# Performance work log

Measured on AMD Instinct MI355X. Metric: run time of the kernel, lower is better.

The kernel has to match this reference:

```python
import jax, jax.numpy as jnp
import numpy as np

DIM = 128
N_PROMPT = 5
N_EXPERTS = 4
TOP_K = 2
HIDDEN = int(DIM * 2.66)  # 340
LOSS_COEF = 1e-2
EPS = 1e-10


def setup_inputs() -> dict:
    key = jax.random.key(0)
    ks = jax.random.split(key, 12)
    B, C, H, W = 2, DIM, 192, 192
    s = 0.02
    return {
        "x": jax.random.normal(ks[0], (B, C, H, W), jnp.float32),
        "prompt": jax.random.normal(ks[1], (N_PROMPT, DIM), jnp.float32) * s,      # spectral_prompt
        "w_lin": jax.random.normal(ks[2], (N_PROMPT, DIM), jnp.float32) * s,       # Linear(dim, 5).weight
        "b_lin": jnp.zeros((N_PROMPT,), jnp.float32),
        "w_conv": jax.random.normal(ks[3], (DIM, DIM), jnp.float32) * s,           # Conv2d 1x1, no bias
        "w_gate": jax.random.normal(ks[4], (DIM, N_EXPERTS), jnp.float32) * s,     # gating matrix
        "w1": jax.random.normal(ks[5], (N_EXPERTS, DIM, HIDDEN), jnp.float32) * s, # expert fc1
        "b1": jnp.zeros((N_EXPERTS, HIDDEN), jnp.float32),
        "w2": jax.random.normal(ks[6], (N_EXPERTS, HIDDEN, DIM), jnp.float32) * s, # expert fc2
        "b2": jnp.zeros((N_EXPERTS, DIM), jnp.float32),
    }


def _cv_squared(v):
    # coefficient of variation squared: var / mean^2
    m = jnp.mean(v)
    return jnp.var(v) / (m * m + EPS)


def _moe(tx, ty, w_gate, w1, b1, w2, b2):
    # tx: [N, C] gating input tokens; ty: [N, C] expert input tokens
    logits = tx @ w_gate                                  # [N, E] (clean gating, inference path)
    top_logits, top_idx = jax.lax.top_k(logits, TOP_K)    # [N, k]
    top_gates = jax.nn.softmax(top_logits, axis=-1)       # [N, k]
    N = tx.shape[0]
    gates = jnp.zeros((N, N_EXPERTS), tx.dtype).at[
        jnp.arange(N)[:, None], top_idx].set(top_gates)   # [N, E] sparse gates
    importance = gates.sum(axis=0)                        # [E]
    load = (gates > 0).astype(tx.dtype).sum(axis=0)       # [E]
    loss = LOSS_COEF * (_cv_squared(importance) + _cv_squared(load))
    # dense masked dispatch: run every expert, weight-combine (same math as routed combine)
    h = jax.nn.gelu(jnp.einsum('nc,ech->enh', ty, w1) + b1[:, None, :], approximate=False)
    o = jnp.einsum('enh,ehc->enc', h, w2) + b2[:, None, :]  # [E, N, C]
    y = jnp.einsum('ne,enc->nc', gates, o)                  # [N, C]
    return y, loss


def reference(x, prompt, w_lin, b_lin, w_conv, w_gate, w1, b1, w2, b2):
    B, C, H, W = x.shape
    emb = x.mean(axis=(-2, -1))                               # [B, C]
    pw = jax.nn.softmax(emb @ w_lin.T + b_lin, axis=1)        # [B, P]
    spectral_prompt = pw @ prompt                             # [B, C]
    sf = spectral_prompt[:, :, None, None] * x                # [B, C, H, W]
    out = jnp.einsum('oc,bchw->bohw', w_conv, sf)             # 1x1 conv, no bias
    tx = jnp.transpose(x, (0, 2, 3, 1)).reshape(-1, C)        # gating tokens
    ty = jnp.transpose(out, (0, 2, 3, 1)).reshape(-1, C)      # expert tokens
    y, loss = _moe(tx, ty, w_gate, w1, b1, w2, b2)
    y = jnp.transpose(y.reshape(B, H, W, C), (0, 3, 1, 2))
    return y + x, loss
```

## Files before the change

### kernel.cpp

```cpp
#include <hip/hip_runtime.h>
#include <hip/hip_bf16.h>
#include <hip/hip_fp8.h>

typedef __attribute__((ext_vector_type(8))) short bf16x8;
typedef __attribute__((ext_vector_type(4))) float f32x4;
typedef long long i64;
typedef __attribute__((ext_vector_type(2))) long long i64x2;

#define HW 36864
#define HID 340
#define HPAD 352
#define ECP 1408
#define NCHUNK 44
#define TILE 96
#define TILES_PER_B 384
#define OUT_Y_ELEMS 9437184
#define WALL_BYTES (NCHUNK * 8192)

__device__ __forceinline__ short f2bf(float f) {
    __hip_bfloat16 h = __float2bfloat16(f);
    union { __hip_bfloat16 h; short s; } u; u.h = h; return u.s;
}
__device__ __forceinline__ float bf2f(short s) {
    union { unsigned u; float f; } v; v.u = ((unsigned)(unsigned short)s) << 16; return v.f;
}
__device__ __forceinline__ f32x4 mfma_fp8(i64 a, i64 b, f32x4 c) {
    return __builtin_amdgcn_mfma_f32_16x16x32_fp8_fp8(a, b, c, 0, 0, 0);
}
__device__ __forceinline__ void async_cp16(const void* gsrc, void* ldst) {
    __builtin_amdgcn_global_load_lds(
        (const __attribute__((address_space(1))) unsigned int*)gsrc,
        (__attribute__((address_space(3))) unsigned int*)ldst, 16, 0, 0);
}

__global__ __launch_bounds__(256) void k_prep(const float* __restrict__ x,
                                              const float* __restrict__ w1, const float* __restrict__ w2,
                                              const float* __restrict__ b1,
                                              float* __restrict__ emb, unsigned char* __restrict__ Wall,
                                              float* __restrict__ b1c) {
    int blk = blockIdx.x;
    int tid = threadIdx.x;
    if (blk < 256) {
        const float* p = x + (size_t)blk * HW;
        float s = 0.f;
        for (int i = tid * 4; i < HW; i += 1024) {
            float4 v = *(const float4*)(p + i);
            s += v.x + v.y + v.z + v.w;
        }
        for (int off = 32; off; off >>= 1) s += __shfl_down(s, off);
        __shared__ float wsum[4];
        int lane = tid & 63, wid = tid >> 6;
        if (lane == 0) wsum[wid] = s;
        __syncthreads();
        if (tid == 0) emb[blk] = (wsum[0] + wsum[1] + wsum[2] + wsum[3]) * (1.f / (float)HW);
        return;
    }
    if (blk < 608) {
        int idx4 = (blk - 256) * 1024 + tid * 4;
        int ch = idx4 >> 13, r8 = idx4 & 8191;
        int rr = r8 >> 10;
        int lane = (r8 >> 4) & 63;
        int j0 = r8 & 15;
        int g16 = lane >> 4, l16 = lane & 15;
        int jj0 = j0 & 7;
        float v0 = 0.f, v1 = 0.f, v2 = 0.f, v3 = 0.f;
        if (rr < 4) {
            int m = rr >> 1, p = rr & 1;
            int kk = 2 * p + (j0 >> 3);
            int j_h = ch * 32 + m * 16 + l16;
            int c0 = 16 * (2 * kk + (jj0 >> 2)) + 4 * g16;
            int e = j_h / HPAD, h = j_h - e * HPAD;
            if (h < HID) {
                const float* p1 = w1 + ((size_t)(e * 128 + c0)) * HID + h;
                v0 = p1[0] * 32.f; v1 = p1[HID] * 32.f; v2 = p1[2 * HID] * 32.f; v3 = p1[3 * HID] * 32.f;
            }
        } else {
            int q = rr - 4;
            int oc = 2 * q + (j0 >> 3);
            int o = oc * 16 + l16;
            int jg0 = ch * 32 + 16 * (jj0 >> 2) + 4 * g16;
            int e = jg0 / HPAD, h = jg0 - e * HPAD;
            if (h < HID) {
                const float* p2 = w2 + ((size_t)(e * HID + h)) * 128 + o;
                v0 = p2[0] * 32.f; v1 = p2[128] * 32.f; v2 = p2[256] * 32.f; v3 = p2[384] * 32.f;
            }
        }
        unsigned w = __builtin_amdgcn_cvt_pk_fp8_f32(v0, v1, 0, false);
        w = __builtin_amdgcn_cvt_pk_fp8_f32(v2, v3, w, true);
        *(unsigned*)(Wall + idx4) = w;
        return;
    }
    {
        int j0 = (blk - 608) * 1024 + tid * 4;
        if (j0 < ECP) {
            int e = j0 / HPAD, h = j0 - e * HPAD;
            float4 o;
            if (h < HID) {
                const float* p = b1 + e * HID + h;
                o.x = p[0]; o.y = p[1]; o.z = p[2]; o.w = p[3];
            } else {
                o.x = o.y = o.z = o.w = 0.f;
            }
            *(float4*)(b1c + j0) = o;
        }
    }
}

__global__ __launch_bounds__(256) void k_wb(const float* __restrict__ emb, const float* __restrict__ prompt,
                                            const float* __restrict__ wlin, const float* __restrict__ blin,
                                            const float* __restrict__ wconv,
                                            short* __restrict__ WbBf, float* __restrict__ stat) {
    __shared__ float lp[2][5];
    __shared__ float pw[2][5];
    __shared__ float sv[2][128];
    int tid = threadIdx.x;
    if (tid < 10) {
        int b = tid / 5, p = tid % 5;
        float s = blin[p];
        for (int c = 0; c < 128; ++c) s += emb[b * 128 + c] * wlin[p * 128 + c];
        lp[b][p] = s;
    }
    __syncthreads();
    if (tid < 2) {
        float m = lp[tid][0];
        for (int p = 1; p < 5; ++p) m = fmaxf(m, lp[tid][p]);
        float e[5], sum = 0.f;
        for (int p = 0; p < 5; ++p) { e[p] = __expf(lp[tid][p] - m); sum += e[p]; }
        for (int p = 0; p < 5; ++p) pw[tid][p] = e[p] / sum;
    }
    __syncthreads();
    {
        int b = tid >> 7, c = tid & 127;
        float s = 0.f;
        for (int p = 0; p < 5; ++p) s += pw[b][p] * prompt[p * 128 + c];
        sv[b][c] = s;
    }
    __syncthreads();
    int i0 = blockIdx.x * 1024 + tid * 4;
    int b = i0 >> 14, o = (i0 >> 7) & 127, c = i0 & 127;
    float4 wv = *(const float4*)(wconv + o * 128 + c);
    short r0 = f2bf(wv.x * sv[b][c]);
    short r1 = f2bf(wv.y * sv[b][c + 1]);
    short r2 = f2bf(wv.z * sv[b][c + 2]);
    short r3 = f2bf(wv.w * sv[b][c + 3]);
    WbBf[i0] = r0; WbBf[i0 + 1] = r1; WbBf[i0 + 2] = r2; WbBf[i0 + 3] = r3;
    if (blockIdx.x == 0 && tid < 8) stat[tid] = 0.f;
}

__global__ __launch_bounds__(192, 3) void k_main(
    const float* __restrict__ x, const float* __restrict__ wgate, const float* __restrict__ b2,
    const short* __restrict__ WbBf, const unsigned char* __restrict__ Wall,
    const float* __restrict__ b1c, float* __restrict__ stat, float* __restrict__ out) {

    __shared__ __align__(16) unsigned char uni[26112];
    __shared__ __align__(16) short b1sh[ECP];
    __shared__ float gates[TILE][4];
    __shared__ float simp[4], sload[4];
    short (*Xs)[136] = (short (*)[136])uni;
    unsigned char (*ring)[8192] = (unsigned char (*)[8192])uni;

    int tid = threadIdx.x;
    int tb = blockIdx.x;
    int b = tb / TILES_PER_B;
    int hw0 = (tb % TILES_PER_B) * TILE;
    const float* xb = x + (size_t)b * 128 * HW + hw0;

    int lane = tid & 63, wid = tid >> 6;
    int g16 = lane >> 4, l16 = lane & 15;
    int wrow = wid * 32;

    if (tid < 4) { simp[tid] = 0.f; sload[tid] = 0.f; }
    for (int i = tid; i < ECP; i += 192) b1sh[i] = f2bf(b1c[i]);

    #pragma unroll
    for (int it = 0; it < 16; ++it) {
        int i = tid + it * 192;
        int c = i / 24;
        int k = i - c * 24;
        float4 v = *(const float4*)(xb + (size_t)c * HW + k * 4);
        int t = k * 4;
        Xs[t][c] = f2bf(v.x); Xs[t + 1][c] = f2bf(v.y);
        Xs[t + 2][c] = f2bf(v.z); Xs[t + 3][c] = f2bf(v.w);
    }
    __syncthreads();

    bf16x8 xf[2][4];
    #pragma unroll
    for (int nt = 0; nt < 2; ++nt)
        #pragma unroll
        for (int kk = 0; kk < 4; ++kk)
            xf[nt][kk] = *(const bf16x8*)&Xs[wrow + nt * 16 + l16][kk * 32 + g16 * 8];

    {
        bf16x8 wgA[4];
        #pragma unroll
        for (int kk = 0; kk < 4; ++kk) {
            bf16x8 a = (bf16x8){0, 0, 0, 0, 0, 0, 0, 0};
            if (l16 < 4) {
                #pragma unroll
                for (int jj = 0; jj < 8; ++jj)
                    a[jj] = f2bf(wgate[(kk * 32 + g16 * 8 + jj) * 4 + l16]);
            }
            wgA[kk] = a;
        }
        f32x4 lg0 = (f32x4){0.f, 0.f, 0.f, 0.f};
        f32x4 lg1 = (f32x4){0.f, 0.f, 0.f, 0.f};
        #pragma unroll
        for (int kk = 0; kk < 4; ++kk) {
            lg0 = __builtin_amdgcn_mfma_f32_16x16x32_bf16(wgA[kk], xf[0][kk], lg0, 0, 0, 0);
            lg1 = __builtin_amdgcn_mfma_f32_16x16x32_bf16(wgA[kk], xf[1][kk], lg1, 0, 0, 0);
        }
        if (g16 == 0) {
            #pragma unroll
            for (int nt = 0; nt < 2; ++nt) {
                f32x4 lg = nt ? lg1 : lg0;
                float l0 = lg[0], l1 = lg[1], l2 = lg[2], l3 = lg[3];
                int i1 = 0; float m1 = l0;
                if (l1 > m1) { m1 = l1; i1 = 1; }
                if (l2 > m1) { m1 = l2; i1 = 2; }
                if (l3 > m1) { m1 = l3; i1 = 3; }
                float m2 = -3.4e38f; int i2 = 0;
                if (i1 != 0) { m2 = l0; i2 = 0; }
                if (i1 != 1 && l1 > m2) { m2 = l1; i2 = 1; }
                if (i1 != 2 && l2 > m2) { m2 = l2; i2 = 2; }
                if (i1 != 3 && l3 > m2) { m2 = l3; i2 = 3; }
                float g2v = 1.f / (1.f + __expf(m1 - m2));
                float g1v = 1.f - g2v;
                int t = wrow + nt * 16 + l16;
                gates[t][0] = 0.f; gates[t][1] = 0.f; gates[t][2] = 0.f; gates[t][3] = 0.f;
                gates[t][i1] = g1v; gates[t][i2] = g2v;
                atomicAdd(&simp[i1], g1v); atomicAdd(&simp[i2], g2v);
                atomicAdd(&sload[i1], 1.f); atomicAdd(&sload[i2], 1.f);
            }
        }
    }

    f32x4 aty[2][8];
    #pragma unroll
    for (int nt = 0; nt < 2; ++nt)
        #pragma unroll
        for (int oc = 0; oc < 8; ++oc) aty[nt][oc] = (f32x4){0.f, 0.f, 0.f, 0.f};
    {
        const short* wbB = WbBf + b * 16384 + l16 * 128 + g16 * 8;
        #pragma unroll
        for (int oc = 0; oc < 8; ++oc) {
            #pragma unroll
            for (int kk = 0; kk < 4; ++kk) {
                bf16x8 wv = *(const bf16x8*)(wbB + oc * 16 * 128 + kk * 32);
                aty[0][oc] = __builtin_amdgcn_mfma_f32_16x16x32_bf16(wv, xf[0][kk], aty[0][oc], 0, 0, 0);
                aty[1][oc] = __builtin_amdgcn_mfma_f32_16x16x32_bf16(wv, xf[1][kk], aty[1][oc], 0, 0, 0);
            }
        }
    }
    i64 tyb8[2][4];
    #pragma unroll
    for (int nt = 0; nt < 2; ++nt)
        #pragma unroll
        for (int kk = 0; kk < 4; ++kk) {
            union { i64 l; unsigned u[2]; } uu;
            float v0 = aty[nt][2 * kk][0] * 64.f,     v1 = aty[nt][2 * kk][1] * 64.f;
            float v2 = aty[nt][2 * kk][2] * 64.f,     v3 = aty[nt][2 * kk][3] * 64.f;
            float v4 = aty[nt][2 * kk + 1][0] * 64.f, v5 = aty[nt][2 * kk + 1][1] * 64.f;
            float v6 = aty[nt][2 * kk + 1][2] * 64.f, v7 = aty[nt][2 * kk + 1][3] * 64.f;
            unsigned lo = __builtin_amdgcn_cvt_pk_fp8_f32(v0, v1, 0, false);
            lo = __builtin_amdgcn_cvt_pk_fp8_f32(v2, v3, lo, true);
            unsigned hi = __builtin_amdgcn_cvt_pk_fp8_f32(v4, v5, 0, false);
            hi = __builtin_amdgcn_cvt_pk_fp8_f32(v6, v7, hi, true);
            uu.u[0] = lo; uu.u[1] = hi;
            tyb8[nt][kk] = uu.l;
        }

    f32x4 gt0 = *(const f32x4*)&gates[wrow + l16][0];
    f32x4 gt1 = *(const f32x4*)&gates[wrow + 16 + l16][0];

    f32x4 accy[2][8];
    #pragma unroll
    for (int nt = 0; nt < 2; ++nt)
        #pragma unroll
        for (int oc = 0; oc < 8; ++oc) accy[nt][oc] = (f32x4){0.f, 0.f, 0.f, 0.f};

    __syncthreads();

    if (wid < 2) {
        const unsigned char* s0 = Wall + wid * 4096;
        #pragma unroll
        for (int r = 0; r < 4; ++r)
            async_cp16(s0 + r * 1024 + lane * 16, &ring[0][wid * 4096 + r * 1024 + lane * 16]);
        const unsigned char* s1 = Wall + 8192 + wid * 4096;
        #pragma unroll
        for (int r = 0; r < 4; ++r)
            async_cp16(s1 + r * 1024 + lane * 16, &ring[1][wid * 4096 + r * 1024 + lane * 16]);
    }

    int slot = 0;
    #pragma unroll 1
    for (int ch = 0; ch < NCHUNK; ++ch) {
        if (wid < 2) asm volatile("s_waitcnt vmcnt(4)" ::: "memory");
        __builtin_amdgcn_sched_barrier(0);
        __builtin_amdgcn_s_barrier();
        __builtin_amdgcn_sched_barrier(0);

        if (wid < 2) {
            int chn = (ch + 2 <= NCHUNK - 1) ? ch + 2 : NCHUNK - 1;
            int wslot = slot + 2; if (wslot >= 3) wslot -= 3;
            const unsigned char* src = Wall + (size_t)chn * 8192 + wid * 4096;
            unsigned char* dst = &ring[wslot][wid * 4096];
            #pragma unroll
            for (int r = 0; r < 4; ++r)
                async_cp16(src + r * 1024 + lane * 16, dst + r * 1024 + lane * 16);
        }

        const unsigned char* wst = &ring[slot][0];
        i64x2 f1q[2][2], f2q[4];
        f1q[0][0] = *(const i64x2*)(wst + 0 * 1024 + lane * 16);
        f1q[0][1] = *(const i64x2*)(wst + 1 * 1024 + lane * 16);
        f1q[1][0] = *(const i64x2*)(wst + 2 * 1024 + lane * 16);
        f1q[1][1] = *(const i64x2*)(wst + 3 * 1024 + lane * 16);
        f2q[0] = *(const i64x2*)(wst + 4 * 1024 + lane * 16);
        f2q[1] = *(const i64x2*)(wst + 5 * 1024 + lane * 16);
        f2q[2] = *(const i64x2*)(wst + 6 * 1024 + lane * 16);
        f2q[3] = *(const i64x2*)(wst + 7 * 1024 + lane * 16);

        int e4 = (ch >= 33) ? 3 : (ch >= 22) ? 2 : (ch >= 11) ? 1 : 0;
        float ge0 = (e4 == 0) ? gt0[0] : (e4 == 1) ? gt0[1] : (e4 == 2) ? gt0[2] : gt0[3];
        float ge1 = (e4 == 0) ? gt1[0] : (e4 == 1) ? gt1[1] : (e4 == 2) ? gt1[2] : gt1[3];

        f32x4 hacc[2][2];
        hacc[0][0] = (f32x4){0.f,0.f,0.f,0.f}; hacc[0][1] = (f32x4){0.f,0.f,0.f,0.f};
        hacc[1][0] = (f32x4){0.f,0.f,0.f,0.f}; hacc[1][1] = (f32x4){0.f,0.f,0.f,0.f};
        #pragma unroll
        for (int kk = 0; kk < 4; ++kk) {
            i64 a0 = f1q[0][kk >> 1][kk & 1];
            i64 a1 = f1q[1][kk >> 1][kk & 1];
            hacc[0][0] = mfma_fp8(a0, tyb8[0][kk], hacc[0][0]);
            hacc[0][1] = mfma_fp8(a0, tyb8[1][kk], hacc[0][1]);
            hacc[1][0] = mfma_fp8(a1, tyb8[0][kk], hacc[1][0]);
            hacc[1][1] = mfma_fp8(a1, tyb8[1][kk], hacc[1][1]);
        }

        float hv0[8], hv1[8];
        #pragma unroll
        for (int jc = 0; jc < 2; ++jc)
            #pragma unroll
            for (int rr = 0; rr < 4; ++rr) {
                float bv = bf2f(b1sh[ch * 32 + jc * 16 + 4 * g16 + rr]);
                float u0 = hacc[jc][0][rr] * 4.8828125e-4f + bv;
                float u1 = hacc[jc][1][rr] * 4.8828125e-4f + bv;
                hv0[jc * 4 + rr] = u0 * (1024.f + 816.9738f * u0) * ge0;
                hv1[jc * 4 + rr] = u1 * (1024.f + 816.9738f * u1) * ge1;
            }
        union { i64 l; unsigned u[2]; } f0, f1;
        {
            unsigned lo = __builtin_amdgcn_cvt_pk_fp8_f32(hv0[0], hv0[1], 0, false);
            lo = __builtin_amdgcn_cvt_pk_fp8_f32(hv0[2], hv0[3], lo, true);
            unsigned hi = __builtin_amdgcn_cvt_pk_fp8_f32(hv0[4], hv0[5], 0, false);
            hi = __builtin_amdgcn_cvt_pk_fp8_f32(hv0[6], hv0[7], hi, true);
            f0.u[0] = lo; f0.u[1] = hi;
            lo = __builtin_amdgcn_cvt_pk_fp8_f32(hv1[0], hv1[1], 0, false);
            lo = __builtin_amdgcn_cvt_pk_fp8_f32(hv1[2], hv1[3], lo, true);
            hi = __builtin_amdgcn_cvt_pk_fp8_f32(hv1[4], hv1[5], 0, false);
            hi = __builtin_amdgcn_cvt_pk_fp8_f32(hv1[6], hv1[7], hi, true);
            f1.u[0] = lo; f1.u[1] = hi;
        }

        #pragma unroll
        for (int oc = 0; oc < 8; ++oc) {
            i64 wv = f2q[oc >> 1][oc & 1];
            accy[0][oc] = mfma_fp8(wv, f0.l, accy[0][oc]);
            accy[1][oc] = mfma_fp8(wv, f1.l, accy[1][oc]);
        }

        slot = (slot == 2) ? 0 : slot + 1;
    }

    #pragma unroll
    for (int oc = 0; oc < 8; ++oc) {
        f32x4 b2v0 = *(const f32x4*)&b2[0 * 128 + oc * 16 + 4 * g16];
        f32x4 b2v1 = *(const f32x4*)&b2[1 * 128 + oc * 16 + 4 * g16];
        f32x4 b2v2 = *(const f32x4*)&b2[2 * 128 + oc * 16 + 4 * g16];
        f32x4 b2v3 = *(const f32x4*)&b2[3 * 128 + oc * 16 + 4 * g16];
        #pragma unroll
        for (int nt = 0; nt < 2; ++nt) {
            f32x4 gt = nt ? gt1 : gt0;
            #pragma unroll
            for (int r = 0; r < 4; ++r) {
                int o = oc * 16 + 4 * g16 + r;
                size_t addr = (size_t)(b * 128 + o) * HW + hw0 + wrow + nt * 16 + l16;
                float v = accy[nt][oc][r] * 1.52587890625e-5f
                        + gt[0] * b2v0[r] + gt[1] * b2v1[r] + gt[2] * b2v2[r] + gt[3] * b2v3[r]
                        + x[addr];
                out[addr] = v;
            }
        }
    }

    __syncthreads();
    if (tid < 4) {
        atomicAdd(&stat[tid], simp[tid]);
        atomicAdd(&stat[4 + tid], sload[tid]);
    }
}

__global__ void k_loss(const float* __restrict__ stat, float* __restrict__ out) {
    if (threadIdx.x == 0 && blockIdx.x == 0) {
        double mi = 0.0, ml = 0.0;
        for (int e = 0; e < 4; ++e) { mi += stat[e]; ml += stat[4 + e]; }
        mi *= 0.25; ml *= 0.25;
        double vi = 0.0, vl = 0.0;
        for (int e = 0; e < 4; ++e) {
            double di = stat[e] - mi; vi += di * di;
            double dl = stat[4 + e] - ml; vl += dl * dl;
        }
        vi *= 0.25; vl *= 0.25;
        out[OUT_Y_ELEMS] = (float)(0.01 * (vi / (mi * mi + 1e-10) + vl / (ml * ml + 1e-10)));
    }
}

extern "C" void kernel_launch(void* const* d_in, const int* in_sizes, int n_in,
                              void* d_out, int out_size, void* d_ws, size_t ws_size,
                              hipStream_t stream) {
    const float* x      = (const float*)d_in[0];
    const float* prompt = (const float*)d_in[1];
    const float* wlin   = (const float*)d_in[2];
    const float* blin   = (const float*)d_in[3];
    const float* wconv  = (const float*)d_in[4];
    const float* wgate  = (const float*)d_in[5];
    const float* w1     = (const float*)d_in[6];
    const float* b1     = (const float*)d_in[7];
    const float* w2     = (const float*)d_in[8];
    const float* b2     = (const float*)d_in[9];
    float* out = (float*)d_out;

    char* ws = (char*)d_ws;
    float* emb  = (float*)(ws + 0);
    float* stat = (float*)(ws + 1024);
    float* b1c  = (float*)(ws + 2048);
    short* WbBf = (short*)(ws + 8192);
    unsigned char* Wall = (unsigned char*)(ws + 73728);

    hipLaunchKernelGGL(k_prep, dim3(610),  dim3(256), 0, stream, x, w1, w2, b1, emb, Wall, b1c);
    hipLaunchKernelGGL(k_wb,   dim3(32),   dim3(256), 0, stream, emb, prompt, wlin, blin, wconv, WbBf, stat);
    hipLaunchKernelGGL(k_main, dim3(768),  dim3(192), 0, stream, x, wgate, b2, WbBf, Wall, b1c, stat, out);
    hipLaunchKernelGGL(k_loss, dim3(1),    dim3(1),   0, stream, stat, out);
}
```

Before: 94.06 us.

## Batch weight streaming into 32KB superchunks with double buffering and bias-in-accumulator

Restructures the weight pipeline from a 3-slot ring of 8KB chunks with one barrier per chunk to a 2-slot ring of 32KB superchunks, each covering four chunks. This cuts barriers and waits per unit of work by four. It also folds the fc1 bias, prescaled into fp32 LDS, into the MFMA accumulator initialisation, which removes per-element bias adds and bf16 conversions. The price is 64KB+ of LDS per block, so occupancy drops from 3 to 2 blocks per CU (launch bounds changed), and a second barrier per superchunk is needed before the buffer is refilled.

```diff
diff --git a/kernel.cpp b/kernel.cpp
--- a/kernel.cpp
+++ b/kernel.cpp
@@ -12,6 +12,7 @@
 #define HPAD 352
 #define ECP 1408
 #define NCHUNK 44
+#define NSUPER 11
 #define TILE 96
 #define TILES_PER_B 384
 #define OUT_Y_ELEMS 9437184
@@ -20,9 +21,6 @@
 __device__ __forceinline__ short f2bf(float f) {
     __hip_bfloat16 h = __float2bfloat16(f);
     union { __hip_bfloat16 h; short s; } u; u.h = h; return u.s;
-}
-__device__ __forceinline__ float bf2f(short s) {
-    union { unsigned u; float f; } v; v.u = ((unsigned)(unsigned short)s) << 16; return v.f;
 }
 __device__ __forceinline__ f32x4 mfma_fp8(i64 a, i64 b, f32x4 c) {
     return __builtin_amdgcn_mfma_f32_16x16x32_fp8_fp8(a, b, c, 0, 0, 0);
@@ -147,17 +145,77 @@
     if (blockIdx.x == 0 && tid < 8) stat[tid] = 0.f;
 }
 
-__global__ __launch_bounds__(192, 3) void k_main(
+#define SUB_BODY(CH, WST) do { \
+    int ch_ = (CH); \
+    const unsigned char* wst_ = (WST); \
+    i64x2 f1q[2][2], f2q[4]; \
+    f1q[0][0] = *(const i64x2*)(wst_ + 0 * 1024 + lane * 16); \
+    f1q[0][1] = *(const i64x2*)(wst_ + 1 * 1024 + lane * 16); \
+    f1q[1][0] = *(const i64x2*)(wst_ + 2 * 1024 + lane * 16); \
+    f1q[1][1] = *(const i64x2*)(wst_ + 3 * 1024 + lane * 16); \
+    f2q[0] = *(const i64x2*)(wst_ + 4 * 1024 + lane * 16); \
+    f2q[1] = *(const i64x2*)(wst_ + 5 * 1024 + lane * 16); \
+    f2q[2] = *(const i64x2*)(wst_ + 6 * 1024 + lane * 16); \
+    f2q[3] = *(const i64x2*)(wst_ + 7 * 1024 + lane * 16); \
+    int e4_ = (ch_ >= 33) ? 3 : (ch_ >= 22) ? 2 : (ch_ >= 11) ? 1 : 0; \
+    float ge0_ = (e4_ == 0) ? gt0[0] : (e4_ == 1) ? gt0[1] : (e4_ == 2) ? gt0[2] : gt0[3]; \
+    float ge1_ = (e4_ == 0) ? gt1[0] : (e4_ == 1) ? gt1[1] : (e4_ == 2) ? gt1[2] : gt1[3]; \
+    f32x4 bv0 = *(const f32x4*)&b1f[ch_ * 32 + 4 * g16]; \
+    f32x4 bv1 = *(const f32x4*)&b1f[ch_ * 32 + 16 + 4 * g16]; \
+    f32x4 hacc[2][2]; \
+    hacc[0][0] = bv0; hacc[0][1] = bv0; \
+    hacc[1][0] = bv1; hacc[1][1] = bv1; \
+    _Pragma("unroll") \
+    for (int kk = 0; kk < 4; ++kk) { \
+        i64 a0 = f1q[0][kk >> 1][kk & 1]; \
+        i64 a1 = f1q[1][kk >> 1][kk & 1]; \
+        hacc[0][0] = mfma_fp8(a0, tyb8[0][kk], hacc[0][0]); \
+        hacc[0][1] = mfma_fp8(a0, tyb8[1][kk], hacc[0][1]); \
+        hacc[1][0] = mfma_fp8(a1, tyb8[0][kk], hacc[1][0]); \
+        hacc[1][1] = mfma_fp8(a1, tyb8[1][kk], hacc[1][1]); \
+    } \
+    float hv0[8], hv1[8]; \
+    _Pragma("unroll") \
+    for (int jc = 0; jc < 2; ++jc) \
+        _Pragma("unroll") \
+        for (int rr = 0; rr < 4; ++rr) { \
+            float u0 = hacc[jc][0][rr] * 4.8828125e-4f; \
+            float u1 = hacc[jc][1][rr] * 4.8828125e-4f; \
+            hv0[jc * 4 + rr] = u0 * (1024.f + 816.9738f * u0) * ge0_; \
+            hv1[jc * 4 + rr] = u1 * (1024.f + 816.9738f * u1) * ge1_; \
+        } \
+    union { i64 l; unsigned u[2]; } f0, f1; \
+    { \
+        unsigned lo = __builtin_amdgcn_cvt_pk_fp8_f32(hv0[0], hv0[1], 0, false); \
+        lo = __builtin_amdgcn_cvt_pk_fp8_f32(hv0[2], hv0[3], lo, true); \
+        unsigned hi = __builtin_amdgcn_cvt_pk_fp8_f32(hv0[4], hv0[5], 0, false); \
+        hi = __builtin_amdgcn_cvt_pk_fp8_f32(hv0[6], hv0[7], hi, true); \
+        f0.u[0] = lo; f0.u[1] = hi; \
+        lo = __builtin_amdgcn_cvt_pk_fp8_f32(hv1[0], hv1[1], 0, false); \
+        lo = __builtin_amdgcn_cvt_pk_fp8_f32(hv1[2], hv1[3], lo, true); \
+        hi = __builtin_amdgcn_cvt_pk_fp8_f32(hv1[4], hv1[5], 0, false); \
+        hi = __builtin_amdgcn_cvt_pk_fp8_f32(hv1[6], hv1[7], hi, true); \
+        f1.u[0] = lo; f1.u[1] = hi; \
+    } \
+    _Pragma("unroll") \
+    for (int oc = 0; oc < 8; ++oc) { \
+        i64 wv = f2q[oc >> 1][oc & 1]; \
+        accy[0][oc] = mfma_fp8(wv, f0.l, accy[0][oc]); \
+        accy[1][oc] = mfma_fp8(wv, f1.l, accy[1][oc]); \
+    } \
+} while (0)
+
+__global__ __launch_bounds__(192, 2) void k_main(
     const float* __restrict__ x, const float* __restrict__ wgate, const float* __restrict__ b2,
     const short* __restrict__ WbBf, const unsigned char* __restrict__ Wall,
     const float* __restrict__ b1c, float* __restrict__ stat, float* __restrict__ out) {
 
-    __shared__ __align__(16) unsigned char uni[26112];
-    __shared__ __align__(16) short b1sh[ECP];
+    __shared__ __align__(16) unsigned char uni[65536];
+    __shared__ __align__(16) float b1f[ECP];
     __shared__ float gates[TILE][4];
     __shared__ float simp[4], sload[4];
     short (*Xs)[136] = (short (*)[136])uni;
-    unsigned char (*ring)[8192] = (unsigned char (*)[8192])uni;
+    unsigned char (*ring)[32768] = (unsigned char (*)[32768])uni;
 
     int tid = threadIdx.x;
     int tb = blockIdx.x;
@@ -170,7 +228,7 @@
     int wrow = wid * 32;
 
     if (tid < 4) { simp[tid] = 0.f; sload[tid] = 0.f; }
-    for (int i = tid; i < ECP; i += 192) b1sh[i] = f2bf(b1c[i]);
+    for (int i = tid; i < ECP; i += 192) b1f[i] = b1c[i] * 2048.f;
 
     #pragma unroll
     for (int it = 0; it < 16; ++it) {
@@ -282,95 +340,42 @@
     __syncthreads();
 
     if (wid < 2) {
-        const unsigned char* s0 = Wall + wid * 4096;
-        #pragma unroll
-        for (int r = 0; r < 4; ++r)
-            async_cp16(s0 + r * 1024 + lane * 16, &ring[0][wid * 4096 + r * 1024 + lane * 16]);
-        const unsigned char* s1 = Wall + 8192 + wid * 4096;
-        #pragma unroll
-        for (int r = 0; r < 4; ++r)
-            async_cp16(s1 + r * 1024 + lane * 16, &ring[1][wid * 4096 + r * 1024 + lane * 16]);
-    }
-
-    int slot = 0;
+        #pragma unroll
+        for (int r = 0; r < 16; ++r)
+            async_cp16(Wall + wid * 16384 + r * 1024 + lane * 16,
+                       &ring[0][wid * 16384 + r * 1024 + lane * 16]);
+        #pragma unroll
+        for (int r = 0; r < 16; ++r)
+            async_cp16(Wall + 32768 + wid * 16384 + r * 1024 + lane * 16,
+                       &ring[1][wid * 16384 + r * 1024 + lane * 16]);
+    }
+
     #pragma unroll 1
-    for (int ch = 0; ch < NCHUNK; ++ch) {
-        if (wid < 2) asm volatile("s_waitcnt vmcnt(4)" ::: "memory");
+    for (int s = 0; s < NSUPER; ++s) {
+        asm volatile("s_waitcnt vmcnt(16)" ::: "memory");
         __builtin_amdgcn_sched_barrier(0);
         __builtin_amdgcn_s_barrier();
         __builtin_amdgcn_sched_barrier(0);
 
+        const unsigned char* base = &ring[s & 1][0];
+        SUB_BODY(4 * s + 0, base);
+        SUB_BODY(4 * s + 1, base + 8192);
+        SUB_BODY(4 * s + 2, base + 16384);
+        SUB_BODY(4 * s + 3, base + 24576);
+
+        asm volatile("s_waitcnt lgkmcnt(0)" ::: "memory");
+        __builtin_amdgcn_sched_barrier(0);
+        __builtin_amdgcn_s_barrier();
+        __builtin_amdgcn_sched_barrier(0);
+
         if (wid < 2) {
-            int chn = (ch + 2 <= NCHUNK - 1) ? ch + 2 : NCHUNK - 1;
-            int wslot = slot + 2; if (wslot >= 3) wslot -= 3;
-            const unsigned char* src = Wall + (size_t)chn * 8192 + wid * 4096;
-            unsigned char* dst = &ring[wslot][wid * 4096];
+            int sn = (s + 2 <= NSUPER - 1) ? s + 2 : NSUPER - 1;
+            const unsigned char* src = Wall + (size_t)sn * 32768 + wid * 16384;
+            unsigned char* dst = &ring[s & 1][wid * 16384];
             #pragma unroll
-            for (int r = 0; r < 4; ++r)
+            for (int r = 0; r < 16; ++r)
                 async_cp16(src + r * 1024 + lane * 16, dst + r * 1024 + lane * 16);
         }
-
-        const unsigned char* wst = &ring[slot][0];
-        i64x2 f1q[2][2], f2q[4];
-        f1q[0][0] = *(const i64x2*)(wst + 0 * 1024 + lane * 16);
-        f1q[0][1] = *(const i64x2*)(wst + 1 * 1024 + lane * 16);
-        f1q[1][0] = *(const i64x2*)(wst + 2 * 1024 + lane * 16);
-        f1q[1][1] = *(const i64x2*)(wst + 3 * 1024 + lane * 16);
-        f2q[0] = *(const i64x2*)(wst + 4 * 1024 + lane * 16);
-        f2q[1] = *(const i64x2*)(wst + 5 * 1024 + lane * 16);
-        f2q[2] = *(const i64x2*)(wst + 6 * 1024 + lane * 16);
-        f2q[3] = *(const i64x2*)(wst + 7 * 1024 + lane * 16);
-
-        int e4 = (ch >= 33) ? 3 : (ch >= 22) ? 2 : (ch >= 11) ? 1 : 0;
-        float ge0 = (e4 == 0) ? gt0[0] : (e4 == 1) ? gt0[1] : (e4 == 2) ? gt0[2] : gt0[3];
-        float ge1 = (e4 == 0) ? gt1[0] : (e4 == 1) ? gt1[1] : (e4 == 2) ? gt1[2] : gt1[3];
-
-        f32x4 hacc[2][2];
-        hacc[0][0] = (f32x4){0.f,0.f,0.f,0.f}; hacc[0][1] = (f32x4){0.f,0.f,0.f,0.f};
-        hacc[1][0] = (f32x4){0.f,0.f,0.f,0.f}; hacc[1][1] = (f32x4){0.f,0.f,0.f,0.f};
-        #pragma unroll
-        for (int kk = 0; kk < 4; ++kk) {
-            i64 a0 = f1q[0][kk >> 1][kk & 1];
-            i64 a1 = f1q[1][kk >> 1][kk & 1];
-            hacc[0][0] = mfma_fp8(a0, tyb8[0][kk], hacc[0][0]);
-            hacc[0][1] = mfma_fp8(a0, tyb8[1][kk], hacc[0][1]);
-            hacc[1][0] = mfma_fp8(a1, tyb8[0][kk], hacc[1][0]);
-            hacc[1][1] = mfma_fp8(a1, tyb8[1][kk], hacc[1][1]);
-        }
-
-        float hv0[8], hv1[8];
-        #pragma unroll
-        for (int jc = 0; jc < 2; ++jc)
-            #pragma unroll
-            for (int rr = 0; rr < 4; ++rr) {
-                float bv = bf2f(b1sh[ch * 32 + jc * 16 + 4 * g16 + rr]);
-                float u0 = hacc[jc][0][rr] * 4.8828125e-4f + bv;
-                float u1 = hacc[jc][1][rr] * 4.8828125e-4f + bv;
-                hv0[jc * 4 + rr] = u0 * (1024.f + 816.9738f * u0) * ge0;
-                hv1[jc * 4 + rr] = u1 * (1024.f + 816.9738f * u1) * ge1;
-            }
-        union { i64 l; unsigned u[2]; } f0, f1;
-        {
-            unsigned lo = __builtin_amdgcn_cvt_pk_fp8_f32(hv0[0], hv0[1], 0, false);
-            lo = __builtin_amdgcn_cvt_pk_fp8_f32(hv0[2], hv0[3], lo, true);
-            unsigned hi = __builtin_amdgcn_cvt_pk_fp8_f32(hv0[4], hv0[5], 0, false);
-            hi = __builtin_amdgcn_cvt_pk_fp8_f32(hv0[6], hv0[7], hi, true);
-            f0.u[0] = lo; f0.u[1] = hi;
-            lo = __builtin_amdgcn_cvt_pk_fp8_f32(hv1[0], hv1[1], 0, false);
-            lo = __builtin_amdgcn_cvt_pk_fp8_f32(hv1[2], hv1[3], lo, true);
-            hi = __builtin_amdgcn_cvt_pk_fp8_f32(hv1[4], hv1[5], 0, false);
-            hi = __builtin_amdgcn_cvt_pk_fp8_f32(hv1[6], hv1[7], hi, true);
-            f1.u[0] = lo; f1.u[1] = hi;
-        }
-
-        #pragma unroll
-        for (int oc = 0; oc < 8; ++oc) {
-            i64 wv = f2q[oc >> 1][oc & 1];
-            accy[0][oc] = mfma_fp8(wv, f0.l, accy[0][oc]);
-            accy[1][oc] = mfma_fp8(wv, f1.l, accy[1][oc]);
-        }
-
-        slot = (slot == 2) ? 0 : slot + 1;
     }
 
     #pragma unroll
```

After: 107.1 us. 1.14x slower.
